# Performance work log

Hardware: AMD Instinct MI355X
Metric: run time of the kernel (lower is better)

The kernel has to match this reference:

```python
import jax, jax.numpy as jnp
import numpy as np
import math

DIM = 1024
HEADS = 16
HEAD_DIM = DIM // HEADS
FFN = 4096
B, S = 2, 2048
EPS = 1e-12


def layernorm(x, w, b):
    u = jnp.mean(x, axis=-1, keepdims=True)
    s = jnp.mean((x - u) ** 2, axis=-1, keepdims=True)
    return w * ((x - u) / jnp.sqrt(s + EPS)) + b


def setup_inputs() -> dict:
    key = jax.random.key(0)
    ks = jax.random.split(key, 8)
    scale = 0.02
    return {
        "x": jax.random.normal(ks[0], (B, S, DIM), dtype=jnp.float32),
        "mask": jnp.zeros((1, 1, S, S), dtype=jnp.float32),
        "wq": jax.random.normal(ks[1], (DIM, DIM), dtype=jnp.float32) * scale,
        "wk": jax.random.normal(ks[2], (DIM, DIM), dtype=jnp.float32) * scale,
        "wv": jax.random.normal(ks[3], (DIM, DIM), dtype=jnp.float32) * scale,
        "wo": jax.random.normal(ks[4], (DIM, DIM), dtype=jnp.float32) * scale,
        "w1": jax.random.normal(ks[5], (DIM, FFN), dtype=jnp.float32) * scale,
        "w2": jax.random.normal(ks[6], (FFN, DIM), dtype=jnp.float32) * scale,
        "ln1_w": jnp.ones((DIM,), dtype=jnp.float32),
        "ln1_b": jnp.zeros((DIM,), dtype=jnp.float32),
        "ln2_w": jnp.ones((DIM,), dtype=jnp.float32),
        "ln2_b": jnp.zeros((DIM,), dtype=jnp.float32),
    }


def reference(x, mask, wq, wk, wv, wo, w1, w2, ln1_w, ln1_b, ln2_w, ln2_b):
    # --- attention sub-block (pre-LN) ---
    h = layernorm(x, ln1_w, ln1_b)
    q = (h @ wq).reshape(B, S, HEADS, HEAD_DIM).transpose(0, 2, 1, 3)  # [B,H,S,D]
    k = (h @ wk).reshape(B, S, HEADS, HEAD_DIM).transpose(0, 2, 1, 3)
    v = (h @ wv).reshape(B, S, HEADS, HEAD_DIM).transpose(0, 2, 1, 3)
    scores = jnp.einsum("bhsd,bhtd->bhst", q, k) / math.sqrt(HEAD_DIM)
    scores = scores + mask
    probs = jax.nn.softmax(scores.astype(jnp.float32), axis=-1).astype(q.dtype)
    attn = jnp.einsum("bhst,bhtd->bhsd", probs, v)  # [B,H,S,D]
    attn = attn.transpose(0, 2, 1, 3).reshape(B, S, DIM)
    x = x + attn @ wo
    # --- FFN sub-block (pre-LN) ---
    h = layernorm(x, ln2_w, ln2_b)
    m = jax.nn.gelu(h @ w1, approximate=False) @ w2
    return x + m
```

## Files before the change

kernel.cpp:

```cpp
#include <hip/hip_runtime.h>
#include <math.h>


#define DIMSZ 1024
#define SEQ   2048
#define BATCH 2
#define NHEAD 16
#define HD    64
#define FFNSZ 4096
#define ROWS  (BATCH*SEQ)
#define KSPLIT 2
#define KRANGE (SEQ/KSPLIT)

typedef __attribute__((ext_vector_type(8))) short bf8_t;
typedef __attribute__((ext_vector_type(4))) float f4_t;

__device__ __forceinline__ unsigned short f2bf(float f) {
  union { float f; unsigned u; } c; c.f = f;
  unsigned u = c.u;
  return (unsigned short)((u + 0x7fffu + ((u >> 16) & 1u)) >> 16);
}

__device__ __forceinline__ float bf2f(unsigned short u) {
  union { unsigned u; float f; } c; c.u = ((unsigned)u) << 16; return c.f;
}

__device__ __forceinline__ float fast_exp2(float x) {
#if __has_builtin(__builtin_amdgcn_exp2f)
  return __builtin_amdgcn_exp2f(x);
#else
  return exp2f(x);
#endif
}

__device__ __forceinline__ float fast_rcp(float x) {
#if __has_builtin(__builtin_amdgcn_rcpf)
  return __builtin_amdgcn_rcpf(x);
#else
  return 1.f / x;
#endif
}

__device__ __forceinline__ float gelu_fast(float x) {
  float ax = fabsf(x) * 0.70710678118654752f;
  float t  = fast_rcp(fmaf(0.3275911f, ax, 1.f));
  float p  = fmaf(t, 1.061405429f, -1.453152027f);
  p = fmaf(t, p, 1.421413741f);
  p = fmaf(t, p, -0.284496736f);
  p = fmaf(t, p, 0.254829592f);
  p = p * t;
  float e  = fast_exp2(-ax * ax * 1.4426950408889634f);
  float er = fmaf(-p, e, 1.f);
  er = copysignf(er, x);
  return 0.5f * x * (1.f + er);
}

__device__ __forceinline__ unsigned int pk_trunc_bf16(float a, float b) {
#if __has_builtin(__builtin_amdgcn_perm)
  return __builtin_amdgcn_perm(__float_as_uint(b), __float_as_uint(a), 0x07060302u);
#else
  return (__float_as_uint(b) & 0xffff0000u) | (__float_as_uint(a) >> 16);
#endif
}

__device__ __forceinline__ void async16(const void* g, void* l) {
  __builtin_amdgcn_global_load_lds((const __attribute__((address_space(1))) void*)g,
                                   (__attribute__((address_space(3))) void*)l,
                                   16, 0, 0);
}

__device__ __forceinline__ f4_t mfma_bf16(bf8_t a, bf8_t b, f4_t c) {
  return __builtin_amdgcn_mfma_f32_16x16x32_bf16(a, b, c, 0, 0, 0);
}

__global__ __launch_bounds__(256) void prep_kernel(
    const float* __restrict__ x,  const float* __restrict__ ln1w,
    const float* __restrict__ ln1b, unsigned short* __restrict__ h1,
    const float* __restrict__ wq, const float* __restrict__ wk,
    const float* __restrict__ wv, const float* __restrict__ wo,
    const float* __restrict__ w1, const float* __restrict__ w2,
    unsigned short* __restrict__ wqkvT, unsigned short* __restrict__ woT,
    unsigned short* __restrict__ w1T,   unsigned short* __restrict__ w2T) {
  __shared__ float t[32][33];
  int id = blockIdx.x;
  if (id >= 12288) {
    int row  = (id - 12288) * 4 + (threadIdx.x >> 6);
    int lane = threadIdx.x & 63;
    const float4* xr = (const float4*)(x + (size_t)row * DIMSZ);
    float4 v[4];
    float s = 0.f, s2 = 0.f;
#pragma unroll
    for (int i = 0; i < 4; ++i) {
      v[i] = xr[lane + 64*i];
      s  += (v[i].x + v[i].y) + (v[i].z + v[i].w);
      s2 += (v[i].x*v[i].x + v[i].y*v[i].y) + (v[i].z*v[i].z + v[i].w*v[i].w);
    }
#pragma unroll
    for (int off = 32; off; off >>= 1) {
      s  += __shfl_xor(s,  off);
      s2 += __shfl_xor(s2, off);
    }
    float mean = s * (1.f/DIMSZ);
    float var  = s2 * (1.f/DIMSZ) - mean*mean;
    float rstd = rsqrtf(var + 1e-12f);
#pragma unroll
    for (int i = 0; i < 4; ++i) {
      float4 wv4 = ((const float4*)ln1w)[lane + 64*i];
      float4 bv4 = ((const float4*)ln1b)[lane + 64*i];
      ushort4 o;
      o.x = f2bf((v[i].x - mean) * rstd * wv4.x + bv4.x);
      o.y = f2bf((v[i].y - mean) * rstd * wv4.y + bv4.y);
      o.z = f2bf((v[i].z - mean) * rstd * wv4.z + bv4.z);
      o.w = f2bf((v[i].w - mean) * rstd * wv4.w + bv4.w);
      *(ushort4*)(h1 + (size_t)row * DIMSZ + (size_t)(lane + 64*i) * 4) = o;
    }
    return;
  }
  const float* w; unsigned short* wT; int K, N, n0, k0;
  if (id < 4096) {
    int wsel = id >> 10, tt = id & 1023;
    K = 1024; N = 1024;
    n0 = (tt & 31) * 32; k0 = (tt >> 5) * 32;
    w  = (wsel == 0) ? wq : (wsel == 1) ? wk : (wsel == 2) ? wv : wo;
    wT = (wsel == 0) ? wqkvT : (wsel == 1) ? wqkvT + 1024*1024
       : (wsel == 2) ? wqkvT + 2*1024*1024 : woT;
  } else if (id < 8192) {
    int tt = id - 4096;
    K = 1024; N = 4096;
    n0 = (tt & 127) * 32; k0 = (tt >> 7) * 32;
    w = w1; wT = w1T;
  } else {
    int tt = id - 8192;
    K = 4096; N = 1024;
    n0 = (tt & 31) * 32; k0 = (tt >> 5) * 32;
    w = w2; wT = w2T;
  }
  int tx = threadIdx.x & 31, ty = threadIdx.x >> 5;
#pragma unroll
  for (int i = 0; i < 4; ++i)
    t[ty + 8*i][tx] = w[(size_t)(k0 + ty + 8*i) * N + n0 + tx];
  __syncthreads();
#pragma unroll
  for (int i = 0; i < 4; ++i)
    wT[(size_t)(n0 + ty + 8*i) * K + k0 + tx] = f2bf(t[tx][ty + 8*i]);
}

__global__ __launch_bounds__(256) void ln_kernel(const float* __restrict__ x,
                                                 const float* __restrict__ w,
                                                 const float* __restrict__ b,
                                                 unsigned short* __restrict__ out) {
  int row  = blockIdx.x * 4 + (threadIdx.x >> 6);
  int lane = threadIdx.x & 63;
  const float4* xr = (const float4*)(x + (size_t)row * DIMSZ);
  float4 v[4];
  float s = 0.f, s2 = 0.f;
#pragma unroll
  for (int i = 0; i < 4; ++i) {
    v[i] = xr[lane + 64*i];
    s  += (v[i].x + v[i].y) + (v[i].z + v[i].w);
    s2 += (v[i].x*v[i].x + v[i].y*v[i].y) + (v[i].z*v[i].z + v[i].w*v[i].w);
  }
#pragma unroll
  for (int off = 32; off; off >>= 1) {
    s  += __shfl_xor(s,  off);
    s2 += __shfl_xor(s2, off);
  }
  float mean = s * (1.f/DIMSZ);
  float var  = s2 * (1.f/DIMSZ) - mean*mean;
  float rstd = rsqrtf(var + 1e-12f);
#pragma unroll
  for (int i = 0; i < 4; ++i) {
    float4 wv = ((const float4*)w)[lane + 64*i];
    float4 bv = ((const float4*)b)[lane + 64*i];
    ushort4 o;
    o.x = f2bf((v[i].x - mean) * rstd * wv.x + bv.x);
    o.y = f2bf((v[i].y - mean) * rstd * wv.y + bv.y);
    o.z = f2bf((v[i].z - mean) * rstd * wv.z + bv.z);
    o.w = f2bf((v[i].w - mean) * rstd * wv.w + bv.w);
    *(ushort4*)(out + (size_t)row * DIMSZ + (size_t)(lane + 64*i) * 4) = o;
  }
}

__global__ __launch_bounds__(256) void vt_kernel(const unsigned short* __restrict__ qkv,
                                                 unsigned short* __restrict__ vt) {
  __shared__ unsigned short tile[64][65];
  int bh = blockIdx.y, b = bh >> 4, h = bh & 15;
  int s0 = blockIdx.x * 64;
  int tx = threadIdx.x & 63, ty = threadIdx.x >> 6;
#pragma unroll
  for (int i = 0; i < 16; ++i) {
    int s = ty + i*4;
    tile[s][tx] = qkv[((size_t)(b*SEQ) + s0 + s) * 3072 + 2048 + h*HD + tx];
  }
  __syncthreads();
#pragma unroll
  for (int i = 0; i < 16; ++i) {
    int d = ty + i*4;
    vt[((size_t)bh * HD + d) * SEQ + s0 + tx] = tile[tx][d];
  }
}

template<int EPI, int NT>
__global__ __launch_bounds__(256) void gemm_bt(const unsigned short* __restrict__ A,
                                               const unsigned short* __restrict__ Bt,
                                               void* __restrict__ Cv,
                                               const float* __restrict__ res,
                                               int M, int N, int K, int klen) {
  constexpr int JT = NT / 32;
  __shared__ unsigned short As[2][128][32];
  __shared__ unsigned short Bs[2][NT][32];
  int tid  = threadIdx.x;
  int wv   = tid >> 6, lane = tid & 63, quad = lane >> 4, ml = lane & 15;
  int wrow = (wv >> 1) * 64, wcol = (wv & 1) * (NT/2);
  const unsigned short* Ab = A  + (size_t)blockIdx.y * 128 * K;
  const unsigned short* Bb = Bt + (size_t)blockIdx.x * NT  * K;
  int kbeg = blockIdx.z * klen;
  size_t zoff = (size_t)blockIdx.z * M * N;

  f4_t acc[4][JT];
#pragma unroll
  for (int i = 0; i < 4; ++i)
#pragma unroll
    for (int j = 0; j < JT; ++j) acc[i][j] = (f4_t){0.f, 0.f, 0.f, 0.f};

  int r0 = tid >> 2, c0 = (tid & 3) * 8;

  for (int k0 = kbeg; k0 < kbeg + klen; k0 += 64) {
#pragma unroll
    for (int h = 0; h < 2; ++h) {
      const unsigned short* ap = Ab + (size_t)r0 * K + k0 + h*32 + c0;
      async16(ap,          &As[h][r0][c0]);
      async16(ap + 64*K,   &As[h][r0 + 64][c0]);
      const unsigned short* bp = Bb + (size_t)r0 * K + k0 + h*32 + c0;
      async16(bp,          &Bs[h][r0][c0]);
      if constexpr (NT == 128)
        async16(bp + 64*K, &Bs[h][r0 + 64][c0]);
    }
    __syncthreads();

#pragma unroll
    for (int h = 0; h < 2; ++h) {
      bf8_t af[4], bfr[JT];
#pragma unroll
      for (int i = 0; i < 4; ++i)
        af[i] = *(const bf8_t*)(&As[h][wrow + i*16 + ml][quad * 8]);
#pragma unroll
      for (int j = 0; j < JT; ++j)
        bfr[j] = *(const bf8_t*)(&Bs[h][wcol + j*16 + ml][quad * 8]);
#pragma unroll
      for (int i = 0; i < 4; ++i)
#pragma unroll
        for (int j = 0; j < JT; ++j)
          acc[i][j] = mfma_bf16(bfr[j], af[i], acc[i][j]);
    }
    __syncthreads();
  }

#pragma unroll
  for (int i = 0; i < 4; ++i) {
    int m = blockIdx.y * 128 + wrow + i*16 + ml;
#pragma unroll
    for (int j = 0; j < JT; ++j) {
      int n = blockIdx.x * NT + wcol + j*16 + quad*4;
      size_t off = (size_t)m * N + n;
      if constexpr (EPI == 2) {
        float4 rv = *(const float4*)(res + off);
        float4 ov;
        ov.x = rv.x + acc[i][j][0];
        ov.y = rv.y + acc[i][j][1];
        ov.z = rv.z + acc[i][j][2];
        ov.w = rv.w + acc[i][j][3];
        *(float4*)((float*)Cv + off) = ov;
      } else {
        float v0 = acc[i][j][0], v1 = acc[i][j][1], v2 = acc[i][j][2], v3 = acc[i][j][3];
        if constexpr (EPI == 1) {
          v0 = gelu_fast(v0); v1 = gelu_fast(v1);
          v2 = gelu_fast(v2); v3 = gelu_fast(v3);
        }
        ushort4 o;
        o.x = f2bf(v0); o.y = f2bf(v1); o.z = f2bf(v2); o.w = f2bf(v3);
        *(ushort4*)((unsigned short*)Cv + zoff + off) = o;
      }
    }
  }
}

__global__ __launch_bounds__(256) void w2_combine(const unsigned short* __restrict__ p0,
                                                  const unsigned short* __restrict__ p1,
                                                  const float* __restrict__ x2,
                                                  float* __restrict__ out) {
  size_t t = ((size_t)blockIdx.x * 256 + threadIdx.x) * 4;
  ushort4 a = *(const ushort4*)(p0 + t);
  ushort4 c = *(const ushort4*)(p1 + t);
  float4 r  = *(const float4*)(x2 + t);
  float4 o;
  o.x = r.x + bf2f(a.x) + bf2f(c.x);
  o.y = r.y + bf2f(a.y) + bf2f(c.y);
  o.z = r.z + bf2f(a.z) + bf2f(c.z);
  o.w = r.w + bf2f(a.w) + bf2f(c.w);
  *(float4*)(out + t) = o;
}

__global__ __launch_bounds__(256) void attn_part(const unsigned short* __restrict__ qkv,
                                                 const unsigned short* __restrict__ vt,
                                                 const float* __restrict__ mask,
                                                 unsigned short* __restrict__ pbuf,
                                                 float* __restrict__ lbuf) {
  __shared__ unsigned short Ks[2][64][32];
  __shared__ unsigned short Vs[2][64][32];
  __shared__ unsigned short Ps[4][2][16][72];

  int kz = blockIdx.y;
  int bh = blockIdx.z, b = bh >> 4, h = bh & 15;
  int tid = threadIdx.x;
  int wv = tid >> 6, lane = tid & 63;
  int quad = lane >> 4, ml = lane & 15;
  int q0 = blockIdx.x * 128;
  int qA = q0 + wv * 32 + ml;
  int qB = qA + 16;
  int kbeg = kz * KRANGE;

  const unsigned short* qrowA = qkv + ((size_t)(b*SEQ) + qA) * 3072 + h*HD;
  const unsigned short* qrowB = qkv + ((size_t)(b*SEQ) + qB) * 3072 + h*HD;
  bf8_t qf[2][2];
  qf[0][0] = *(const bf8_t*)(qrowA + quad*8);
  qf[0][1] = *(const bf8_t*)(qrowA + 32 + quad*8);
  qf[1][0] = *(const bf8_t*)(qrowB + quad*8);
  qf[1][1] = *(const bf8_t*)(qrowB + 32 + quad*8);

  const unsigned short* kbase = qkv + ((size_t)(b*SEQ) + kbeg) * 3072 + DIMSZ + h*HD;
  const unsigned short* vbase = vt + (size_t)bh * HD * SEQ + kbeg;
  const float* mrowA = mask + (size_t)qA * SEQ + kbeg;
  const float* mrowB = mask + (size_t)qB * SEQ + kbeg;

  int srow = tid >> 2;
  int scol = (tid & 3) * 8;

  f4_t O[2][4];
#pragma unroll
  for (int g = 0; g < 2; ++g)
#pragma unroll
    for (int dt = 0; dt < 4; ++dt) O[g][dt] = (f4_t){0.f, 0.f, 0.f, 0.f};
  float lR[2] = {0.f, 0.f};

  const float C1 = 0.18033688011112042f;
  const float C2 = 1.4426950408889634f;

  for (int t0 = 0; t0 < KRANGE; t0 += 64) {
    float4 mvA[4], mvB[4];
#pragma unroll
    for (int mt = 0; mt < 4; ++mt) {
      mvA[mt] = *(const float4*)(mrowA + t0 + mt*16 + quad*4);
      mvB[mt] = *(const float4*)(mrowB + t0 + mt*16 + quad*4);
    }

    __syncthreads();
#pragma unroll
    for (int dh = 0; dh < 2; ++dh)
      async16(kbase + (size_t)(t0 + srow) * 3072 + dh*32 + scol,
              &Ks[dh][0][0] + (size_t)tid * 8);
#pragma unroll
    for (int kc = 0; kc < 2; ++kc)
      async16(vbase + (size_t)srow * SEQ + t0 + kc*32 + scol,
              &Vs[kc][0][0] + (size_t)tid * 8);
    __syncthreads();

#pragma unroll
    for (int mt = 0; mt < 4; ++mt) {
      bf8_t kf0 = *(const bf8_t*)(&Ks[0][mt*16 + ml][quad*8]);
      bf8_t kf1 = *(const bf8_t*)(&Ks[1][mt*16 + ml][quad*8]);
#pragma unroll
      for (int g = 0; g < 2; ++g) {
        f4_t s = (f4_t){0.f, 0.f, 0.f, 0.f};
        s = mfma_bf16(kf0, qf[g][0], s);
        s = mfma_bf16(kf1, qf[g][1], s);
        const float4& mv = g ? mvB[mt] : mvA[mt];
        float p0 = fast_exp2(fmaf(s[0], C1, mv.x * C2));
        float p1 = fast_exp2(fmaf(s[1], C1, mv.y * C2));
        float p2 = fast_exp2(fmaf(s[2], C1, mv.z * C2));
        float p3 = fast_exp2(fmaf(s[3], C1, mv.w * C2));
        lR[g] += (p0 + p1) + (p2 + p3);
        uint2 pk;
        pk.x = pk_trunc_bf16(p0, p1);
        pk.y = pk_trunc_bf16(p2, p3);
        *(uint2*)(&Ps[wv][g][ml][mt*16 + quad*4]) = pk;
      }
    }

#pragma unroll
    for (int kc = 0; kc < 2; ++kc) {
      bf8_t pfA = *(const bf8_t*)(&Ps[wv][0][ml][kc*32 + quad*8]);
      bf8_t pfB = *(const bf8_t*)(&Ps[wv][1][ml][kc*32 + quad*8]);
#pragma unroll
      for (int dt = 0; dt < 4; ++dt) {
        bf8_t vf = *(const bf8_t*)(&Vs[kc][dt*16 + ml][quad*8]);
        O[0][dt] = mfma_bf16(vf, pfA, O[0][dt]);
        O[1][dt] = mfma_bf16(vf, pfB, O[1][dt]);
      }
    }
  }

#pragma unroll
  for (int g = 0; g < 2; ++g) {
    lR[g] += __shfl_xor(lR[g], 16);
    lR[g] += __shfl_xor(lR[g], 32);
    int q = g ? qB : qA;
    size_t pb = ((size_t)(bh * KSPLIT + kz) * SEQ + q) * HD;
#pragma unroll
    for (int dt = 0; dt < 4; ++dt) {
      ushort4 o;
      o.x = f2bf(O[g][dt][0]);
      o.y = f2bf(O[g][dt][1]);
      o.z = f2bf(O[g][dt][2]);
      o.w = f2bf(O[g][dt][3]);
      *(ushort4*)(pbuf + pb + dt*16 + quad*4) = o;
    }
    if (quad == 0)
      lbuf[(size_t)(bh * KSPLIT + kz) * SEQ + q] = lR[g];
  }
}

__global__ __launch_bounds__(256) void attn_combine(const unsigned short* __restrict__ pbuf,
                                                    const float* __restrict__ lbuf,
                                                    unsigned short* __restrict__ attno) {
  int t = blockIdx.x * 256 + threadIdx.x;
  int dchunk = t & 15;
  int q = (t >> 4) & (SEQ - 1);
  int bh = t >> 15;
  int b = bh >> 4, h = bh & 15;
  size_t o0 = ((size_t)(bh * KSPLIT + 0) * SEQ + q) * HD + dchunk * 4;
  size_t o1 = ((size_t)(bh * KSPLIT + 1) * SEQ + q) * HD + dchunk * 4;
  ushort4 a = *(const ushort4*)(pbuf + o0);
  ushort4 c = *(const ushort4*)(pbuf + o1);
  float l = lbuf[(size_t)(bh * KSPLIT + 0) * SEQ + q]
          + lbuf[(size_t)(bh * KSPLIT + 1) * SEQ + q];
  float inv = 1.f / l;
  ushort4 o;
  o.x = f2bf((bf2f(a.x) + bf2f(c.x)) * inv);
  o.y = f2bf((bf2f(a.y) + bf2f(c.y)) * inv);
  o.z = f2bf((bf2f(a.z) + bf2f(c.z)) * inv);
  o.w = f2bf((bf2f(a.w) + bf2f(c.w)) * inv);
  *(ushort4*)(attno + ((size_t)(b*SEQ) + q) * DIMSZ + h*HD + dchunk*4) = o;
}

extern "C" void kernel_launch(void* const* d_in, const int* in_sizes, int n_in,
                              void* d_out, int out_size, void* d_ws, size_t ws_size,
                              hipStream_t stream) {
  const float* x    = (const float*)d_in[0];
  const float* mask = (const float*)d_in[1];
  const float* wq   = (const float*)d_in[2];
  const float* wk   = (const float*)d_in[3];
  const float* wvp  = (const float*)d_in[4];
  const float* wo   = (const float*)d_in[5];
  const float* w1   = (const float*)d_in[6];
  const float* w2   = (const float*)d_in[7];
  const float* ln1w = (const float*)d_in[8];
  const float* ln1b = (const float*)d_in[9];
  const float* ln2w = (const float*)d_in[10];
  const float* ln2b = (const float*)d_in[11];
  float* out = (float*)d_out;

  char* ws = (char*)d_ws;
  unsigned short* wqkvT  = (unsigned short*)(ws + 0);
  unsigned short* woT    = (unsigned short*)(ws + 6291456);
  unsigned short* w1T    = (unsigned short*)(ws + 8388608);
  unsigned short* w2T    = (unsigned short*)(ws + 16777216);
  unsigned short* attno  = (unsigned short*)(ws + 25165824);
  float*          x2     = (float*)         (ws + 33554432);
  unsigned short* hbuf   = (unsigned short*)(ws + 50331648);
  unsigned short* qkvb   = (unsigned short*)(ws + 58720256);
  unsigned short* vtb    = (unsigned short*)(ws + 83886080);
  unsigned short* gbuf   = (unsigned short*)(ws + 58720256);
  unsigned short* pbuf   = (unsigned short*)(ws + 33554432);
  float*          lbuf   = (float*)         (ws + 50331648);
  unsigned short* w2p    = (unsigned short*)(ws + 0);

  prep_kernel<<<13312, 256, 0, stream>>>(x, ln1w, ln1b, hbuf,
      wq, wk, wvp, wo, w1, w2,
      wqkvT, woT, w1T, w2T);
  gemm_bt<0,128><<<dim3(3072/128, 4096/128, 1), 256, 0, stream>>>(hbuf, wqkvT, qkvb, nullptr, ROWS, 3072, 1024, 1024);
  vt_kernel<<<dim3(SEQ/64, BATCH*NHEAD), 256, 0, stream>>>(qkvb, vtb);
  attn_part<<<dim3(SEQ/128, KSPLIT, BATCH*NHEAD), 256, 0, stream>>>(qkvb, vtb, mask, pbuf, lbuf);
  attn_combine<<<(BATCH*NHEAD*SEQ*(HD/4))/256, 256, 0, stream>>>(pbuf, lbuf, attno);
  gemm_bt<2,64><<<dim3(1024/64, 4096/128, 1), 256, 0, stream>>>(attno, woT, x2, x, ROWS, 1024, 1024, 1024);
  ln_kernel<<<ROWS/4, 256, 0, stream>>>(x2, ln2w, ln2b, hbuf);
  gemm_bt<1,128><<<dim3(4096/128, 4096/128, 1), 256, 0, stream>>>(hbuf, w1T, gbuf, nullptr, ROWS, FFNSZ, 1024, 1024);
  gemm_bt<0,64><<<dim3(1024/64, 4096/128, 2), 256, 0, stream>>>(gbuf, w2T, w2p, nullptr, ROWS, 1024, 4096, 2048);
  w2_combine<<<(ROWS*DIMSZ/4)/256, 256, 0, stream>>>(w2p, w2p + (size_t)ROWS*DIMSZ, x2, out);

  (void)in_sizes; (void)n_in; (void)out_size; (void)ws_size;
}
```

Measured before the change: 401.7 us.

## Split W2 GEMM four ways with 128x128 tiles and remap attention grid

The W2 projection becomes a dedicated split-K kernel with 128x128 tiles and four K-slices (1024 each). Each slice writes bf16 partials to a separate workspace region, and the combine step sums four partials plus the residual. The intent is more reuse per tile while keeping enough blocks to fill the GPU, at the cost of more partial-sum traffic and extra bf16 rounding. The attention kernel grid is also flattened so consecutive blocks cover different heads and K-splits of the same query block, which may improve cache locality.

```diff
diff --git a/kernel.cpp b/kernel.cpp
--- a/kernel.cpp
+++ b/kernel.cpp
@@ -14,6 +14,8 @@
 
 typedef __attribute__((ext_vector_type(8))) short bf8_t;
 typedef __attribute__((ext_vector_type(4))) float f4_t;
+
+struct Ptr4 { unsigned short *p0, *p1, *p2, *p3; };
 
 __device__ __forceinline__ unsigned short f2bf(float f) {
   union { float f; unsigned u; } c; c.f = f;
@@ -215,7 +217,6 @@
   const unsigned short* Ab = A  + (size_t)blockIdx.y * 128 * K;
   const unsigned short* Bb = Bt + (size_t)blockIdx.x * NT  * K;
   int kbeg = blockIdx.z * klen;
-  size_t zoff = (size_t)blockIdx.z * M * N;
 
   f4_t acc[4][JT];
 #pragma unroll
@@ -279,25 +280,95 @@
         }
         ushort4 o;
         o.x = f2bf(v0); o.y = f2bf(v1); o.z = f2bf(v2); o.w = f2bf(v3);
-        *(ushort4*)((unsigned short*)Cv + zoff + off) = o;
+        *(ushort4*)((unsigned short*)Cv + off) = o;
       }
     }
   }
 }
 
-__global__ __launch_bounds__(256) void w2_combine(const unsigned short* __restrict__ p0,
-                                                  const unsigned short* __restrict__ p1,
+__global__ __launch_bounds__(256) void gemm_bt_split(const unsigned short* __restrict__ A,
+                                                     const unsigned short* __restrict__ Bt,
+                                                     Ptr4 ps,
+                                                     int M, int N, int K, int klen) {
+  constexpr int NT = 128, JT = 4;
+  __shared__ unsigned short As[2][128][32];
+  __shared__ unsigned short Bs[2][NT][32];
+  int tid  = threadIdx.x;
+  int wv   = tid >> 6, lane = tid & 63, quad = lane >> 4, ml = lane & 15;
+  int wrow = (wv >> 1) * 64, wcol = (wv & 1) * (NT/2);
+  const unsigned short* Ab = A  + (size_t)blockIdx.y * 128 * K;
+  const unsigned short* Bb = Bt + (size_t)blockIdx.x * NT  * K;
+  int kbeg = blockIdx.z * klen;
+  unsigned short* C = (blockIdx.z == 0) ? ps.p0 : (blockIdx.z == 1) ? ps.p1
+                    : (blockIdx.z == 2) ? ps.p2 : ps.p3;
+
+  f4_t acc[4][JT];
+#pragma unroll
+  for (int i = 0; i < 4; ++i)
+#pragma unroll
+    for (int j = 0; j < JT; ++j) acc[i][j] = (f4_t){0.f, 0.f, 0.f, 0.f};
+
+  int r0 = tid >> 2, c0 = (tid & 3) * 8;
+
+  for (int k0 = kbeg; k0 < kbeg + klen; k0 += 64) {
+#pragma unroll
+    for (int h = 0; h < 2; ++h) {
+      const unsigned short* ap = Ab + (size_t)r0 * K + k0 + h*32 + c0;
+      async16(ap,          &As[h][r0][c0]);
+      async16(ap + 64*K,   &As[h][r0 + 64][c0]);
+      const unsigned short* bp = Bb + (size_t)r0 * K + k0 + h*32 + c0;
+      async16(bp,          &Bs[h][r0][c0]);
+      async16(bp + 64*K,   &Bs[h][r0 + 64][c0]);
+    }
+    __syncthreads();
+
+#pragma unroll
+    for (int h = 0; h < 2; ++h) {
+      bf8_t af[4], bfr[JT];
+#pragma unroll
+      for (int i = 0; i < 4; ++i)
+        af[i] = *(const bf8_t*)(&As[h][wrow + i*16 + ml][quad * 8]);
+#pragma unroll
+      for (int j = 0; j < JT; ++j)
+        bfr[j] = *(const bf8_t*)(&Bs[h][wcol + j*16 + ml][quad * 8]);
+#pragma unroll
+      for (int i = 0; i < 4; ++i)
+#pragma unroll
+        for (int j = 0; j < JT; ++j)
+          acc[i][j] = mfma_bf16(bfr[j], af[i], acc[i][j]);
+    }
+    __syncthreads();
+  }
+
+#pragma unroll
+  for (int i = 0; i < 4; ++i) {
+    int m = blockIdx.y * 128 + wrow + i*16 + ml;
+#pragma unroll
+    for (int j = 0; j < JT; ++j) {
+      int n = blockIdx.x * NT + wcol + j*16 + quad*4;
+      size_t off = (size_t)m * N + n;
+      ushort4 o;
+      o.x = f2bf(acc[i][j][0]); o.y = f2bf(acc[i][j][1]);
+      o.z = f2bf(acc[i][j][2]); o.w = f2bf(acc[i][j][3]);
+      *(ushort4*)(C + off) = o;
+    }
+  }
+}
+
+__global__ __launch_bounds__(256) void w2_combine(Ptr4 ps,
                                                   const float* __restrict__ x2,
                                                   float* __restrict__ out) {
   size_t t = ((size_t)blockIdx.x * 256 + threadIdx.x) * 4;
-  ushort4 a = *(const ushort4*)(p0 + t);
-  ushort4 c = *(const ushort4*)(p1 + t);
+  ushort4 a = *(const ushort4*)(ps.p0 + t);
+  ushort4 b = *(const ushort4*)(ps.p1 + t);
+  ushort4 c = *(const ushort4*)(ps.p2 + t);
+  ushort4 d = *(const ushort4*)(ps.p3 + t);
   float4 r  = *(const float4*)(x2 + t);
   float4 o;
-  o.x = r.x + bf2f(a.x) + bf2f(c.x);
-  o.y = r.y + bf2f(a.y) + bf2f(c.y);
-  o.z = r.z + bf2f(a.z) + bf2f(c.z);
-  o.w = r.w + bf2f(a.w) + bf2f(c.w);
+  o.x = r.x + (bf2f(a.x) + bf2f(b.x)) + (bf2f(c.x) + bf2f(d.x));
+  o.y = r.y + (bf2f(a.y) + bf2f(b.y)) + (bf2f(c.y) + bf2f(d.y));
+  o.z = r.z + (bf2f(a.z) + bf2f(b.z)) + (bf2f(c.z) + bf2f(d.z));
+  o.w = r.w + (bf2f(a.w) + bf2f(b.w)) + (bf2f(c.w) + bf2f(d.w));
   *(float4*)(out + t) = o;
 }
 
@@ -310,12 +381,15 @@
   __shared__ unsigned short Vs[2][64][32];
   __shared__ unsigned short Ps[4][2][16][72];
 
-  int kz = blockIdx.y;
-  int bh = blockIdx.z, b = bh >> 4, h = bh & 15;
+  int id = blockIdx.x;
+  int g  = id & 63;
+  int kz = g & 1;
+  int bh = g >> 1, b = bh >> 4, h = bh & 15;
+  int qblk = id >> 6;
   int tid = threadIdx.x;
   int wv = tid >> 6, lane = tid & 63;
   int quad = lane >> 4, ml = lane & 15;
-  int q0 = blockIdx.x * 128;
+  int q0 = qblk * 128;
   int qA = q0 + wv * 32 + ml;
   int qB = qA + 16;
   int kbeg = kz * KRANGE;
@@ -338,9 +412,9 @@
 
   f4_t O[2][4];
 #pragma unroll
-  for (int g = 0; g < 2; ++g)
-#pragma unroll
-    for (int dt = 0; dt < 4; ++dt) O[g][dt] = (f4_t){0.f, 0.f, 0.f, 0.f};
+  for (int g2 = 0; g2 < 2; ++g2)
+#pragma unroll
+    for (int dt = 0; dt < 4; ++dt) O[g2][dt] = (f4_t){0.f, 0.f, 0.f, 0.f};
   float lR[2] = {0.f, 0.f};
 
   const float C1 = 0.18033688011112042f;
@@ -370,20 +444,20 @@
       bf8_t kf0 = *(const bf8_t*)(&Ks[0][mt*16 + ml][quad*8]);
       bf8_t kf1 = *(const bf8_t*)(&Ks[1][mt*16 + ml][quad*8]);
 #pragma unroll
-      for (int g = 0; g < 2; ++g) {
+      for (int gg = 0; gg < 2; ++gg) {
         f4_t s = (f4_t){0.f, 0.f, 0.f, 0.f};
-        s = mfma_bf16(kf0, qf[g][0], s);
-        s = mfma_bf16(kf1, qf[g][1], s);
-        const float4& mv = g ? mvB[mt] : mvA[mt];
+        s = mfma_bf16(kf0, qf[gg][0], s);
+        s = mfma_bf16(kf1, qf[gg][1], s);
+        const float4& mv = gg ? mvB[mt] : mvA[mt];
         float p0 = fast_exp2(fmaf(s[0], C1, mv.x * C2));
         float p1 = fast_exp2(fmaf(s[1], C1, mv.y * C2));
         float p2 = fast_exp2(fmaf(s[2], C1, mv.z * C2));
         float p3 = fast_exp2(fmaf(s[3], C1, mv.w * C2));
-        lR[g] += (p0 + p1) + (p2 + p3);
+        lR[gg] += (p0 + p1) + (p2 + p3);
         uint2 pk;
         pk.x = pk_trunc_bf16(p0, p1);
         pk.y = pk_trunc_bf16(p2, p3);
-        *(uint2*)(&Ps[wv][g][ml][mt*16 + quad*4]) = pk;
+        *(uint2*)(&Ps[wv][gg][ml][mt*16 + quad*4]) = pk;
       }
     }
 
@@ -401,22 +475,22 @@
   }
 
 #pragma unroll
-  for (int g = 0; g < 2; ++g) {
-    lR[g] += __shfl_xor(lR[g], 16);
-    lR[g] += __shfl_xor(lR[g], 32);
-    int q = g ? qB : qA;
+  for (int gg = 0; gg < 2; ++gg) {
+    lR[gg] += __shfl_xor(lR[gg], 16);
+    lR[gg] += __shfl_xor(lR[gg], 32);
+    int q = gg ? qB : qA;
     size_t pb = ((size_t)(bh * KSPLIT + kz) * SEQ + q) * HD;
 #pragma unroll
     for (int dt = 0; dt < 4; ++dt) {
       ushort4 o;
-      o.x = f2bf(O[g][dt][0]);
-      o.y = f2bf(O[g][dt][1]);
-      o.z = f2bf(O[g][dt][2]);
-      o.w = f2bf(O[g][dt][3]);
+      o.x = f2bf(O[gg][dt][0]);
+      o.y = f2bf(O[gg][dt][1]);
+      o.z = f2bf(O[gg][dt][2]);
+      o.w = f2bf(O[gg][dt][3]);
       *(ushort4*)(pbuf + pb + dt*16 + quad*4) = o;
     }
     if (quad == 0)
-      lbuf[(size_t)(bh * KSPLIT + kz) * SEQ + q] = lR[g];
+      lbuf[(size_t)(bh * KSPLIT + kz) * SEQ + q] = lR[gg];
   }
 }
 
@@ -473,20 +547,24 @@
   unsigned short* gbuf   = (unsigned short*)(ws + 58720256);
   unsigned short* pbuf   = (unsigned short*)(ws + 33554432);
   float*          lbuf   = (float*)         (ws + 50331648);
-  unsigned short* w2p    = (unsigned short*)(ws + 0);
+  Ptr4 w2p;
+  w2p.p0 = (unsigned short*)(ws + 0);
+  w2p.p1 = (unsigned short*)(ws + 8388608);
+  w2p.p2 = (unsigned short*)(ws + 25165824);
+  w2p.p3 = (unsigned short*)(ws + 50331648);
 
   prep_kernel<<<13312, 256, 0, stream>>>(x, ln1w, ln1b, hbuf,
       wq, wk, wvp, wo, w1, w2,
       wqkvT, woT, w1T, w2T);
   gemm_bt<0,128><<<dim3(3072/128, 4096/128, 1), 256, 0, stream>>>(hbuf, wqkvT, qkvb, nullptr, ROWS, 3072, 1024, 1024);
   vt_kernel<<<dim3(SEQ/64, BATCH*NHEAD), 256, 0, stream>>>(qkvb, vtb);
-  attn_part<<<dim3(SEQ/128, KSPLIT, BATCH*NHEAD), 256, 0, stream>>>(qkvb, vtb, mask, pbuf, lbuf);
+  attn_part<<<(SEQ/128)*KSPLIT*BATCH*NHEAD, 256, 0, stream>>>(qkvb, vtb, mask, pbuf, lbuf);
   attn_combine<<<(BATCH*NHEAD*SEQ*(HD/4))/256, 256, 0, stream>>>(pbuf, lbuf, attno);
   gemm_bt<2,64><<<dim3(1024/64, 4096/128, 1), 256, 0, stream>>>(attno, woT, x2, x, ROWS, 1024, 1024, 1024);
   ln_kernel<<<ROWS/4, 256, 0, stream>>>(x2, ln2w, ln2b, hbuf);
   gemm_bt<1,128><<<dim3(4096/128, 4096/128, 1), 256, 0, stream>>>(hbuf, w1T, gbuf, nullptr, ROWS, FFNSZ, 1024, 1024);
-  gemm_bt<0,64><<<dim3(1024/64, 4096/128, 2), 256, 0, stream>>>(gbuf, w2T, w2p, nullptr, ROWS, 1024, 4096, 2048);
-  w2_combine<<<(ROWS*DIMSZ/4)/256, 256, 0, stream>>>(w2p, w2p + (size_t)ROWS*DIMSZ, x2, out);
+  gemm_bt_split<<<dim3(1024/128, 4096/128, 4), 256, 0, stream>>>(gbuf, w2T, w2p, ROWS, 1024, 4096, 1024);
+  w2_combine<<<(ROWS*DIMSZ/4)/256, 256, 0, stream>>>(w2p, x2, out);
 
   (void)in_sizes; (void)n_in; (void)out_size; (void)ws_size;
 }
```

New measurement: 410.1 us. +2.1%, slower.

## Double-buffer K/V tiles and widen attention blocks to 64 queries per wave

Applied to the files above, without the earlier changes.

Rewrites the attention partial kernel so each wave handles 64 query rows instead of 32, halving K/V staging per query. K/V tiles and mask loads are double-buffered so the next tile's async copies overlap the current tile's MFMA and exp work. The grid is flattened with a block-to-(bh,kz,qblk) mapping and launch bounds request two blocks per CU. This raises register and LDS pressure (larger O accumulators, two mask register sets) and halves the block count, which could limit occupancy.

```diff
diff --git a/kernel.cpp b/kernel.cpp
--- a/kernel.cpp
+++ b/kernel.cpp
@@ -301,122 +301,139 @@
   *(float4*)(out + t) = o;
 }
 
-__global__ __launch_bounds__(256) void attn_part(const unsigned short* __restrict__ qkv,
-                                                 const unsigned short* __restrict__ vt,
-                                                 const float* __restrict__ mask,
-                                                 unsigned short* __restrict__ pbuf,
-                                                 float* __restrict__ lbuf) {
-  __shared__ unsigned short Ks[2][64][32];
-  __shared__ unsigned short Vs[2][64][32];
-  __shared__ unsigned short Ps[4][2][16][72];
-
-  int kz = blockIdx.y;
-  int bh = blockIdx.z, b = bh >> 4, h = bh & 15;
+__global__ __launch_bounds__(256, 2) void attn_part(const unsigned short* __restrict__ qkv,
+                                                    const unsigned short* __restrict__ vt,
+                                                    const float* __restrict__ mask,
+                                                    unsigned short* __restrict__ pbuf,
+                                                    float* __restrict__ lbuf) {
+  __shared__ unsigned short Ks[2][2][64][32];
+  __shared__ unsigned short Vs[2][2][64][32];
+  __shared__ unsigned short Ps[4][4][16][72];
+
+  int id = blockIdx.x;
+  int g  = id & 63;
+  int kz = g & 1;
+  int bh = g >> 1, b = bh >> 4, h = bh & 15;
+  int qblk = id >> 6;
   int tid = threadIdx.x;
   int wv = tid >> 6, lane = tid & 63;
   int quad = lane >> 4, ml = lane & 15;
-  int q0 = blockIdx.x * 128;
-  int qA = q0 + wv * 32 + ml;
-  int qB = qA + 16;
+  int q0 = qblk * 256 + wv * 64;
   int kbeg = kz * KRANGE;
 
-  const unsigned short* qrowA = qkv + ((size_t)(b*SEQ) + qA) * 3072 + h*HD;
-  const unsigned short* qrowB = qkv + ((size_t)(b*SEQ) + qB) * 3072 + h*HD;
-  bf8_t qf[2][2];
-  qf[0][0] = *(const bf8_t*)(qrowA + quad*8);
-  qf[0][1] = *(const bf8_t*)(qrowA + 32 + quad*8);
-  qf[1][0] = *(const bf8_t*)(qrowB + quad*8);
-  qf[1][1] = *(const bf8_t*)(qrowB + 32 + quad*8);
+  bf8_t qf[4][2];
+  const float* mrow[4];
+#pragma unroll
+  for (int f = 0; f < 4; ++f) {
+    int q = q0 + f*16 + ml;
+    const unsigned short* qr = qkv + ((size_t)(b*SEQ) + q) * 3072 + h*HD;
+    qf[f][0] = *(const bf8_t*)(qr + quad*8);
+    qf[f][1] = *(const bf8_t*)(qr + 32 + quad*8);
+    mrow[f] = mask + (size_t)q * SEQ + kbeg;
+  }
 
   const unsigned short* kbase = qkv + ((size_t)(b*SEQ) + kbeg) * 3072 + DIMSZ + h*HD;
   const unsigned short* vbase = vt + (size_t)bh * HD * SEQ + kbeg;
-  const float* mrowA = mask + (size_t)qA * SEQ + kbeg;
-  const float* mrowB = mask + (size_t)qB * SEQ + kbeg;
 
   int srow = tid >> 2;
   int scol = (tid & 3) * 8;
 
-  f4_t O[2][4];
-#pragma unroll
-  for (int g = 0; g < 2; ++g)
-#pragma unroll
-    for (int dt = 0; dt < 4; ++dt) O[g][dt] = (f4_t){0.f, 0.f, 0.f, 0.f};
-  float lR[2] = {0.f, 0.f};
+  f4_t O[4][4];
+#pragma unroll
+  for (int f = 0; f < 4; ++f)
+#pragma unroll
+    for (int dt = 0; dt < 4; ++dt) O[f][dt] = (f4_t){0.f, 0.f, 0.f, 0.f};
+  float lR[4] = {0.f, 0.f, 0.f, 0.f};
 
   const float C1 = 0.18033688011112042f;
   const float C2 = 1.4426950408889634f;
 
-  for (int t0 = 0; t0 < KRANGE; t0 += 64) {
-    float4 mvA[4], mvB[4];
-#pragma unroll
-    for (int mt = 0; mt < 4; ++mt) {
-      mvA[mt] = *(const float4*)(mrowA + t0 + mt*16 + quad*4);
-      mvB[mt] = *(const float4*)(mrowB + t0 + mt*16 + quad*4);
-    }
-
-    __syncthreads();
+  auto stage = [&](int t0, int buf) {
 #pragma unroll
     for (int dh = 0; dh < 2; ++dh)
       async16(kbase + (size_t)(t0 + srow) * 3072 + dh*32 + scol,
-              &Ks[dh][0][0] + (size_t)tid * 8);
+              &Ks[buf][dh][0][0] + (size_t)tid * 8);
 #pragma unroll
     for (int kc = 0; kc < 2; ++kc)
       async16(vbase + (size_t)srow * SEQ + t0 + kc*32 + scol,
-              &Vs[kc][0][0] + (size_t)tid * 8);
-    __syncthreads();
-
+              &Vs[buf][kc][0][0] + (size_t)tid * 8);
+  };
+  auto loadmask = [&](int t0, float4 (*mv)[4]) {
+#pragma unroll
+    for (int f = 0; f < 4; ++f)
+#pragma unroll
+      for (int mt = 0; mt < 4; ++mt)
+        mv[f][mt] = *(const float4*)(mrow[f] + t0 + mt*16 + quad*4);
+  };
+  auto compute = [&](int buf, float4 (*mv)[4]) {
 #pragma unroll
     for (int mt = 0; mt < 4; ++mt) {
-      bf8_t kf0 = *(const bf8_t*)(&Ks[0][mt*16 + ml][quad*8]);
-      bf8_t kf1 = *(const bf8_t*)(&Ks[1][mt*16 + ml][quad*8]);
-#pragma unroll
-      for (int g = 0; g < 2; ++g) {
+      bf8_t kf0 = *(const bf8_t*)(&Ks[buf][0][mt*16 + ml][quad*8]);
+      bf8_t kf1 = *(const bf8_t*)(&Ks[buf][1][mt*16 + ml][quad*8]);
+#pragma unroll
+      for (int f = 0; f < 4; ++f) {
         f4_t s = (f4_t){0.f, 0.f, 0.f, 0.f};
-        s = mfma_bf16(kf0, qf[g][0], s);
-        s = mfma_bf16(kf1, qf[g][1], s);
-        const float4& mv = g ? mvB[mt] : mvA[mt];
-        float p0 = fast_exp2(fmaf(s[0], C1, mv.x * C2));
-        float p1 = fast_exp2(fmaf(s[1], C1, mv.y * C2));
-        float p2 = fast_exp2(fmaf(s[2], C1, mv.z * C2));
-        float p3 = fast_exp2(fmaf(s[3], C1, mv.w * C2));
-        lR[g] += (p0 + p1) + (p2 + p3);
+        s = mfma_bf16(kf0, qf[f][0], s);
+        s = mfma_bf16(kf1, qf[f][1], s);
+        float p0 = fast_exp2(fmaf(s[0], C1, mv[f][mt].x * C2));
+        float p1 = fast_exp2(fmaf(s[1], C1, mv[f][mt].y * C2));
+        float p2 = fast_exp2(fmaf(s[2], C1, mv[f][mt].z * C2));
+        float p3 = fast_exp2(fmaf(s[3], C1, mv[f][mt].w * C2));
+        lR[f] += (p0 + p1) + (p2 + p3);
         uint2 pk;
         pk.x = pk_trunc_bf16(p0, p1);
         pk.y = pk_trunc_bf16(p2, p3);
-        *(uint2*)(&Ps[wv][g][ml][mt*16 + quad*4]) = pk;
+        *(uint2*)(&Ps[wv][f][ml][mt*16 + quad*4]) = pk;
       }
     }
-
 #pragma unroll
     for (int kc = 0; kc < 2; ++kc) {
-      bf8_t pfA = *(const bf8_t*)(&Ps[wv][0][ml][kc*32 + quad*8]);
-      bf8_t pfB = *(const bf8_t*)(&Ps[wv][1][ml][kc*32 + quad*8]);
+      bf8_t pf[4];
+#pragma unroll
+      for (int f = 0; f < 4; ++f)
+        pf[f] = *(const bf8_t*)(&Ps[wv][f][ml][kc*32 + quad*8]);
 #pragma unroll
       for (int dt = 0; dt < 4; ++dt) {
-        bf8_t vf = *(const bf8_t*)(&Vs[kc][dt*16 + ml][quad*8]);
-        O[0][dt] = mfma_bf16(vf, pfA, O[0][dt]);
-        O[1][dt] = mfma_bf16(vf, pfB, O[1][dt]);
+        bf8_t vf = *(const bf8_t*)(&Vs[buf][kc][dt*16 + ml][quad*8]);
+#pragma unroll
+        for (int f = 0; f < 4; ++f)
+          O[f][dt] = mfma_bf16(vf, pf[f], O[f][dt]);
       }
     }
-  }
-
-#pragma unroll
-  for (int g = 0; g < 2; ++g) {
-    lR[g] += __shfl_xor(lR[g], 16);
-    lR[g] += __shfl_xor(lR[g], 32);
-    int q = g ? qB : qA;
+  };
+
+  float4 mv0[4][4], mv1[4][4];
+  stage(0, 0);
+  loadmask(0, mv0);
+
+#pragma unroll 1
+  for (int c = 0; c < KRANGE/64; c += 2) {
+    int t0 = c*64, t1 = t0 + 64, t2 = t0 + 128;
+    __syncthreads();
+    if (t1 < KRANGE) { stage(t1, 1); loadmask(t1, mv1); }
+    compute(0, mv0);
+    __syncthreads();
+    if (t2 < KRANGE) { stage(t2, 0); loadmask(t2, mv0); }
+    compute(1, mv1);
+  }
+
+#pragma unroll
+  for (int f = 0; f < 4; ++f) {
+    lR[f] += __shfl_xor(lR[f], 16);
+    lR[f] += __shfl_xor(lR[f], 32);
+    int q = q0 + f*16 + ml;
     size_t pb = ((size_t)(bh * KSPLIT + kz) * SEQ + q) * HD;
 #pragma unroll
     for (int dt = 0; dt < 4; ++dt) {
       ushort4 o;
-      o.x = f2bf(O[g][dt][0]);
-      o.y = f2bf(O[g][dt][1]);
-      o.z = f2bf(O[g][dt][2]);
-      o.w = f2bf(O[g][dt][3]);
+      o.x = f2bf(O[f][dt][0]);
+      o.y = f2bf(O[f][dt][1]);
+      o.z = f2bf(O[f][dt][2]);
+      o.w = f2bf(O[f][dt][3]);
       *(ushort4*)(pbuf + pb + dt*16 + quad*4) = o;
     }
     if (quad == 0)
-      lbuf[(size_t)(bh * KSPLIT + kz) * SEQ + q] = lR[g];
+      lbuf[(size_t)(bh * KSPLIT + kz) * SEQ + q] = lR[f];
   }
 }
 
@@ -480,7 +497,7 @@
       wqkvT, woT, w1T, w2T);
   gemm_bt<0,128><<<dim3(3072/128, 4096/128, 1), 256, 0, stream>>>(hbuf, wqkvT, qkvb, nullptr, ROWS, 3072, 1024, 1024);
   vt_kernel<<<dim3(SEQ/64, BATCH*NHEAD), 256, 0, stream>>>(qkvb, vtb);
-  attn_part<<<dim3(SEQ/128, KSPLIT, BATCH*NHEAD), 256, 0, stream>>>(qkvb, vtb, mask, pbuf, lbuf);
+  attn_part<<<(SEQ/256)*KSPLIT*BATCH*NHEAD, 256, 0, stream>>>(qkvb, vtb, mask, pbuf, lbuf);
   attn_combine<<<(BATCH*NHEAD*SEQ*(HD/4))/256, 256, 0, stream>>>(pbuf, lbuf, attno);
   gemm_bt<2,64><<<dim3(1024/64, 4096/128, 1), 256, 0, stream>>>(attno, woT, x2, x, ROWS, 1024, 1024, 1024);
   ln_kernel<<<ROWS/4, 256, 0, stream>>>(x2, ln2w, ln2b, hbuf);
```

After: 529.9 us. 1.32x slower.
